# Kernel tuning notes

Hardware: AMD Instinct MI355X
Metric: run time of the kernel (lower is better)

## Reference

```python
import jax, jax.numpy as jnp
import numpy as np

B, S, D, H = 2, 2048, 1024, 16
HD = D // H  # 64


def setup_inputs() -> dict:
    key = jax.random.key(0)
    ks = jax.random.split(key, 10)
    sc = 1.0 / np.sqrt(D)
    return {
        "decoder_hs": jax.random.normal(ks[0], (B, S, D), jnp.float32),
        "encoder_hs": jax.random.normal(ks[1], (B, S, D), jnp.float32),
        "Wq": jax.random.normal(ks[2], (D, D), jnp.float32) * sc,
        "bq": jax.random.normal(ks[3], (D,), jnp.float32) * 0.02,
        "Wk": jax.random.normal(ks[4], (D, D), jnp.float32) * sc,
        "bk": jax.random.normal(ks[5], (D,), jnp.float32) * 0.02,
        "Wv": jax.random.normal(ks[6], (D, D), jnp.float32) * sc,
        "bv": jax.random.normal(ks[7], (D,), jnp.float32) * 0.02,
        "Wp": jax.random.normal(ks[8], (D, D), jnp.float32) * sc,
        "bp": jax.random.normal(ks[9], (D,), jnp.float32) * 0.02,
    }


def reference(decoder_hs, encoder_hs, Wq, bq, Wk, bk, Wv, bv, Wp, bp):
    b, s, d = decoder_hs.shape
    # torch nn.Linear: y = x @ W.T + b, W is [out, in]
    q = decoder_hs @ Wq.T + bq
    k = encoder_hs @ Wk.T + bk
    v = encoder_hs @ Wv.T + bv
    # head split: [b, s, d] -> [b, h, s, hd]
    q = q.reshape(b, s, H, HD).transpose(0, 2, 1, 3)
    k = k.reshape(b, s, H, HD).transpose(0, 2, 1, 3)
    v = v.reshape(b, s, H, HD).transpose(0, 2, 1, 3)
    scale = 1.0 / np.sqrt(HD).astype(np.float32)
    att = jnp.einsum('bhqd,bhkd->bhqk', q, k) * scale
    att = jax.nn.softmax(att, axis=-1)
    y = jnp.einsum('bhqk,bhkd->bhqd', att, v)
    y = y.transpose(0, 2, 1, 3).reshape(b, s, d)
    return y @ Wp.T + bp
```

## Files before the change

kernel.cpp:

```cpp
#include <hip/hip_runtime.h>
#include <hip/hip_bf16.h>
#include <cstdint>
#include <cstddef>

#define BB 2
#define SS 2048
#define DD 1024
#define HH 16
#define HD 64

typedef __attribute__((ext_vector_type(8))) short bf16x8;
typedef __attribute__((ext_vector_type(4))) float f32x4;
typedef __attribute__((ext_vector_type(16))) float f32x16;

#define GLL(g, l) __builtin_amdgcn_global_load_lds( \
    (const __attribute__((address_space(1))) void*)(g), \
    (__attribute__((address_space(3))) void*)(l), 16, 0, 0)

__device__ __forceinline__ short f2bf_fast(float f) {
    uint32_t u = __float_as_uint(f);
    u += 0x7FFF + ((u >> 16) & 1);
    return (short)(u >> 16);
}
__device__ __forceinline__ uint32_t pack_bf2(float a, float b) {
    uint32_t ua = __float_as_uint(a), ub = __float_as_uint(b);
    ua += 0x7FFF + ((ua >> 16) & 1);
    ub += 0x7FFF + ((ub >> 16) & 1);
    return (ua >> 16) | (ub & 0xFFFF0000u);
}
__device__ __forceinline__ uint32_t cvtpk_bf2(float a, float b) {
    uint32_t r;
    asm("v_cvt_pk_bf16_f32 %0, %1, %2" : "=v"(r) : "v"(a), "v"(b));
    return r;
}
__device__ __forceinline__ void pl32swap(uint32_t& a, uint32_t& b) {
    asm("v_permlane32_swap_b32 %0, %1" : "+v"(a), "+v"(b));
}
__device__ __forceinline__ bf16x8 cvt8(const float* __restrict__ p) {
    float4 a = *(const float4*)p;
    float4 b = *(const float4*)(p + 4);
    union { uint32_t d[4]; bf16x8 v; } r;
    r.d[0] = pack_bf2(a.x, a.y);
    r.d[1] = pack_bf2(a.z, a.w);
    r.d[2] = pack_bf2(b.x, b.y);
    r.d[3] = pack_bf2(b.z, b.w);
    return r.v;
}

__global__ __launch_bounds__(256) void cvt6_kernel(
    const float* __restrict__ s0, const float* __restrict__ s1,
    const float* __restrict__ s2, const float* __restrict__ s3,
    const float* __restrict__ s4, const float* __restrict__ s5,
    short* __restrict__ d0, short* __restrict__ d1, short* __restrict__ d2,
    short* __restrict__ d3, short* __restrict__ d4, short* __restrict__ d5)
{
    const int id = blockIdx.x * 256 + threadIdx.x;
    const float* s; short* d; size_t off;
    if (id < 1048576) {
        int e = id >> 19;
        off = (size_t)(id & 524287) * 8;
        s = e ? s1 : s0;  d = e ? d1 : d0;
    } else {
        int j = id - 1048576;
        int w = j >> 17;
        off = (size_t)(j & 131071) * 8;
        s = (w == 0) ? s2 : (w == 1) ? s3 : (w == 2) ? s4 : s5;
        d = (w == 0) ? d2 : (w == 1) ? d3 : (w == 2) ? d4 : d5;
    }
    bf16x8 r = cvt8(s + off);
    *(uint4*)(d + off) = *(uint4*)&r;
}

template<int BF>
__global__ __launch_bounds__(256, 3) void qkv_gemm_kernel(
    const void* __restrict__ dec, const void* __restrict__ enc,
    const void* __restrict__ Wq, const void* __restrict__ Wk,
    const void* __restrict__ Wv,
    const float* __restrict__ bq, const float* __restrict__ bk,
    const float* __restrict__ bv,
    short* __restrict__ Qo, short* __restrict__ Ko, short* __restrict__ Vo)
{
    __shared__ short As[128 * 32];
    __shared__ short Bs[128 * 32];

    const int z = blockIdx.z;
    const void* Xv = (z == 0) ? dec : enc;
    const void* Wp_ = (z == 0) ? Wq : (z == 1) ? Wk : Wv;
    const float* bias = (z == 0) ? bq : (z == 1) ? bk : bv;
    short* Yo = (z == 0) ? Qo : (z == 1) ? Ko : Vo;
    const float qs = (z == 0) ? (0.125f * 1.44269504088896f) : 1.0f;

    const int t = threadIdx.x;
    const int lane = t & 63, wv = t >> 6;
    const int lr = lane & 15, quad = lane >> 4;
    const int wm = wv >> 1, wn = wv & 1;
    const int m0 = blockIdx.y * 128;
    const int n0 = blockIdx.x * 128;
    const int K = DD;

    f32x4 acc[4][4];
    #pragma unroll
    for (int i = 0; i < 4; i++)
        #pragma unroll
        for (int j = 0; j < 4; j++) acc[i][j] = (f32x4){0.f, 0.f, 0.f, 0.f};

    for (int kb = 0; kb < K; kb += 32) {
        __syncthreads();
        if (BF) {
            const short* Xb = (const short*)Xv;
            const short* Wb = (const short*)Wp_;
            #pragma unroll
            for (int c = 0; c < 2; c++) {
                int r0 = wv * 32 + c * 16;
                int r = r0 + (lane >> 2), ch = (lane & 3) * 8;
                GLL(Xb + (size_t)(m0 + r) * K + kb + ch, &As[r0 * 32]);
                GLL(Wb + (size_t)(n0 + r) * K + kb + ch, &Bs[r0 * 32]);
            }
        } else {
            const float* Xf = (const float*)Xv;
            const float* Wf = (const float*)Wp_;
            #pragma unroll
            for (int c = 0; c < 2; c++) {
                int id = t + c * 256;
                int r = id >> 2, c8 = (id & 3) * 8;
                *(bf16x8*)&As[r * 32 + c8] = cvt8(Xf + (size_t)(m0 + r) * K + kb + c8);
                *(bf16x8*)&Bs[r * 32 + c8] = cvt8(Wf + (size_t)(n0 + r) * K + kb + c8);
            }
        }
        __syncthreads();

        bf16x8 af[4], bfr[4];
        #pragma unroll
        for (int mi = 0; mi < 4; mi++)
            af[mi] = *(const bf16x8*)&As[(wm * 64 + mi * 16 + lr) * 32 + quad * 8];
        #pragma unroll
        for (int ni = 0; ni < 4; ni++)
            bfr[ni] = *(const bf16x8*)&Bs[(wn * 64 + ni * 16 + lr) * 32 + quad * 8];
        #pragma unroll
        for (int mi = 0; mi < 4; mi++)
            #pragma unroll
            for (int ni = 0; ni < 4; ni++)
                acc[mi][ni] = __builtin_amdgcn_mfma_f32_16x16x32_bf16(
                    af[mi], bfr[ni], acc[mi][ni], 0, 0, 0);
    }

    if (z < 2) {
        #pragma unroll
        for (int ni = 0; ni < 4; ni++) {
            int col = n0 + wn * 64 + ni * 16 + lr;
            int h = col >> 6, hd = col & 63;
            float bvv = bias[col];
            #pragma unroll
            for (int mi = 0; mi < 4; mi++) {
                #pragma unroll
                for (int r2 = 0; r2 < 4; r2++) {
                    int row = m0 + wm * 64 + mi * 16 + quad * 4 + r2;
                    int b = row >> 11, s = row & 2047;
                    float v = (acc[mi][ni][r2] + bvv) * qs;
                    size_t off = ((size_t)(b * HH + h) * SS + s) * HD + hd;
                    Yo[off] = f2bf_fast(v);
                }
            }
        }
    } else {
        #pragma unroll
        for (int ni = 0; ni < 4; ni++) {
            int col = n0 + wn * 64 + ni * 16 + lr;
            int h = col >> 6, hd = col & 63;
            float bvv = bias[col];
            #pragma unroll
            for (int mi = 0; mi < 4; mi++) {
                int s0 = m0 + wm * 64 + mi * 16 + quad * 4;
                int b = s0 >> 11, s = s0 & 2047;
                union { uint32_t d[2]; } u;
                u.d[0] = pack_bf2(acc[mi][ni][0] + bvv, acc[mi][ni][1] + bvv);
                u.d[1] = pack_bf2(acc[mi][ni][2] + bvv, acc[mi][ni][3] + bvv);
                size_t off = ((size_t)(b * HH + h) * HD + hd) * SS + s;
                *(uint2*)(Yo + off) = *(uint2*)&u;
            }
        }
    }
}

template<int WBF>
__global__ __launch_bounds__(256, 2) void proj_gemm_kernel(
    const short* __restrict__ X,
    const void* __restrict__ W, const float* __restrict__ bias,
    float* __restrict__ Y)
{
    __shared__ short As[64 * 32];
    __shared__ short Bs[128 * 32];

    const int t = threadIdx.x;
    const int lane = t & 63, wv = t >> 6;
    const int lr = lane & 15, quad = lane >> 4;
    const int wm = wv >> 1, wn = wv & 1;
    const int m0 = blockIdx.y * 64;
    const int n0 = blockIdx.x * 128;
    const int K = DD, N = DD;

    f32x4 acc[2][4];
    #pragma unroll
    for (int i = 0; i < 2; i++)
        #pragma unroll
        for (int j = 0; j < 4; j++) acc[i][j] = (f32x4){0.f, 0.f, 0.f, 0.f};

    for (int kb = 0; kb < K; kb += 32) {
        __syncthreads();
        {
            int r0 = wv * 16;
            int r = r0 + (lane >> 2), ch = (lane & 3) * 8;
            GLL(X + (size_t)(m0 + r) * K + kb + ch, &As[r0 * 32]);
        }
        if (WBF) {
            const short* Wb = (const short*)W;
            #pragma unroll
            for (int c = 0; c < 2; c++) {
                int r0 = wv * 32 + c * 16;
                int r = r0 + (lane >> 2), ch = (lane & 3) * 8;
                GLL(Wb + (size_t)(n0 + r) * K + kb + ch, &Bs[r0 * 32]);
            }
        } else {
            const float* Wf = (const float*)W;
            #pragma unroll
            for (int c = 0; c < 2; c++) {
                int id = t + c * 256;
                int r = id >> 2, c8 = (id & 3) * 8;
                *(bf16x8*)&Bs[r * 32 + c8] = cvt8(Wf + (size_t)(n0 + r) * K + kb + c8);
            }
        }
        __syncthreads();

        bf16x8 af[2], bfr[4];
        #pragma unroll
        for (int mi = 0; mi < 2; mi++)
            af[mi] = *(const bf16x8*)&As[(wm * 32 + mi * 16 + lr) * 32 + quad * 8];
        #pragma unroll
        for (int ni = 0; ni < 4; ni++)
            bfr[ni] = *(const bf16x8*)&Bs[(wn * 64 + ni * 16 + lr) * 32 + quad * 8];
        #pragma unroll
        for (int mi = 0; mi < 2; mi++)
            #pragma unroll
            for (int ni = 0; ni < 4; ni++)
                acc[mi][ni] = __builtin_amdgcn_mfma_f32_16x16x32_bf16(
                    af[mi], bfr[ni], acc[mi][ni], 0, 0, 0);
    }

    #pragma unroll
    for (int ni = 0; ni < 4; ni++) {
        int col = n0 + wn * 64 + ni * 16 + lr;
        float bvv = bias[col];
        #pragma unroll
        for (int mi = 0; mi < 2; mi++) {
            #pragma unroll
            for (int r2 = 0; r2 < 4; r2++) {
                int row = m0 + wm * 32 + mi * 16 + quad * 4 + r2;
                Y[(size_t)row * N + col] = acc[mi][ni][r2] + bvv;
            }
        }
    }
}

__global__ __launch_bounds__(256, 2) void attn_kernel(
    const short* __restrict__ Q,
    const short* __restrict__ Kgl,
    const short* __restrict__ Vt_g,
    short* __restrict__ Y)
{
    __shared__ short Ks[2][128][64];
    __shared__ short Vt[2][64][128];

    const int t = threadIdx.x;
    const int lane = t & 63, w = t >> 6;
    const int lq = lane & 31, hf = lane >> 5;
    const int gl = (lq & 7) ^ ((lq >> 3) & 3);

    const int bid = blockIdx.x;
    const int slot = bid >> 3;
    const int bh = ((slot >> 4) << 3) + (bid & 7);
    const int qt = slot & 15;
    const int b = bh >> 4, h = bh & 15;

    const int q = qt * 128 + w * 32 + lq;
    const short* Qp = Q + ((size_t)bh * SS + q) * HD;
    bf16x8 qf[4];
    #pragma unroll
    for (int j = 0; j < 4; j++)
        qf[j] = *(const bf16x8*)(Qp + j * 16 + hf * 8);

    f32x16 o[2];
    #pragma unroll
    for (int i = 0; i < 16; i++) { o[0][i] = 0.f; o[1][i] = 0.f; }
    f32x4 vsum = (f32x4){0.f, 0.f, 0.f, 0.f};

    const short* Kb = Kgl + (size_t)bh * SS * HD;
    const short* Vb = Vt_g + (size_t)bh * HD * SS;

    auto stage = [&](int kt1, int nb) {
        #pragma unroll
        for (int c = 0; c < 4; c++) {
            int r0 = w * 32 + c * 8;
            int r  = r0 + (lane >> 3);
            int g  = (r & 7) ^ ((r >> 3) & 3);
            int sc = ((lane & 7) ^ g) * 8;
            GLL(Kb + (size_t)(kt1 * 128 + r) * 64 + sc, &Ks[nb][r0][0]);
        }
        #pragma unroll
        for (int c = 0; c < 4; c++) {
            int h0 = w * 16 + c * 4;
            int hd = h0 + (lane >> 4);
            int g  = (hd & 7) ^ ((hd >> 3) & 3);
            int s16 = (lane & 15) ^ g;
            GLL(Vb + (size_t)hd * SS + kt1 * 128 + s16 * 8, &Vt[nb][h0][0]);
        }
    };

    stage(0, 0);
    __syncthreads();

    int cur = 0;
    for (int kt = 0; kt < SS / 128; kt++) {
        if (kt + 1 < SS / 128) stage(kt + 1, cur ^ 1);

        bf16x8 pb[4][2];
        #pragma unroll
        for (int s = 0; s < 4; s++) {
            const short* krow = &Ks[cur][s * 32 + lq][0];
            f32x16 sc = (f32x16){0.f,0.f,0.f,0.f,0.f,0.f,0.f,0.f,
                                 0.f,0.f,0.f,0.f,0.f,0.f,0.f,0.f};
            __builtin_amdgcn_s_setprio(1);
            #pragma unroll
            for (int j = 0; j < 4; j++) {
                bf16x8 kf = *(const bf16x8*)&krow[((j * 2 + hf) ^ gl) * 8];
                sc = __builtin_amdgcn_mfma_f32_32x32x16_bf16(kf, qf[j], sc, 0, 0, 0);
            }
            __builtin_amdgcn_s_setprio(0);

            float ev[16];
            #pragma unroll
            for (int i = 0; i < 16; i++) ev[i] = __builtin_amdgcn_exp2f(sc[i]);
            #pragma unroll
            for (int r = 0; r < 4; r++)
                vsum += (f32x4){ev[4*r], ev[4*r+1], ev[4*r+2], ev[4*r+3]};
            uint32_t dw[8];
            #pragma unroll
            for (int i = 0; i < 8; i++) dw[i] = cvtpk_bf2(ev[2*i], ev[2*i+1]);
            pl32swap(dw[0], dw[2]); pl32swap(dw[1], dw[3]);
            pl32swap(dw[4], dw[6]); pl32swap(dw[5], dw[7]);
            union { uint32_t u[4]; bf16x8 v; } f0, f1;
            f0.u[0] = dw[0]; f0.u[1] = dw[1]; f0.u[2] = dw[2]; f0.u[3] = dw[3];
            f1.u[0] = dw[4]; f1.u[1] = dw[5]; f1.u[2] = dw[6]; f1.u[3] = dw[7];
            pb[s][0] = f0.v; pb[s][1] = f1.v;
        }

        __builtin_amdgcn_s_setprio(1);
        #pragma unroll
        for (int ds = 0; ds < 2; ds++) {
            const short* vrow = &Vt[cur][ds * 32 + lq][0];
            #pragma unroll
            for (int s = 0; s < 4; s++)
                #pragma unroll
                for (int c = 0; c < 2; c++) {
                    bf16x8 va = *(const bf16x8*)&vrow[((s * 4 + c * 2 + hf) ^ gl) * 8];
                    o[ds] = __builtin_amdgcn_mfma_f32_32x32x16_bf16(
                        va, pb[s][c], o[ds], 0, 0, 0);
                }
        }
        __builtin_amdgcn_s_setprio(0);

        __syncthreads();
        cur ^= 1;
    }

    float lsum = (vsum[0] + vsum[1]) + (vsum[2] + vsum[3]);
    lsum += __shfl_xor(lsum, 32, 64);
    float inv = 1.0f / lsum;

    short* Yp = Y + ((size_t)b * SS + q) * DD + h * 64 + hf * 4;
    #pragma unroll
    for (int ds = 0; ds < 2; ds++)
        #pragma unroll
        for (int rr = 0; rr < 4; rr++) {
            union { uint32_t d[2]; } u;
            u.d[0] = pack_bf2(o[ds][rr*4+0] * inv, o[ds][rr*4+1] * inv);
            u.d[1] = pack_bf2(o[ds][rr*4+2] * inv, o[ds][rr*4+3] * inv);
            *(uint2*)(Yp + ds * 32 + rr * 8) = *(uint2*)&u;
        }
}

extern "C" void kernel_launch(void* const* d_in, const int* in_sizes, int n_in,
                              void* d_out, int out_size, void* d_ws, size_t ws_size,
                              hipStream_t stream) {
    const float* dec = (const float*)d_in[0];
    const float* enc = (const float*)d_in[1];
    const float* Wq  = (const float*)d_in[2];
    const float* bq  = (const float*)d_in[3];
    const float* Wk  = (const float*)d_in[4];
    const float* bk  = (const float*)d_in[5];
    const float* Wv  = (const float*)d_in[6];
    const float* bv  = (const float*)d_in[7];
    const float* Wp  = (const float*)d_in[8];
    const float* bp  = (const float*)d_in[9];

    const size_t per = (size_t)BB * HH * SS * HD;
    const size_t wsz = (size_t)DD * DD;
    short* ws = (short*)d_ws;
    short* Qb  = ws;
    short* Kb  = ws + per;
    short* Vtb = ws + 2 * per;
    short* Yb  = ws + 3 * per;

    dim3 qkv_grid(DD / 128, (BB * SS) / 128, 3);
    dim3 proj_grid(DD / 128, (BB * SS) / 64);
    const int attn_blocks = BB * HH * (SS / 128);
    const int cvt_blocks = (2 * 524288 + 4 * 131072) / 256;

    const size_t need = (6 * per + 4 * wsz) * sizeof(short);
    if (ws_size >= need) {
        short* decb = ws + 4 * per;
        short* encb = ws + 5 * per;
        short* Wqb  = ws + 6 * per;
        short* Wkb  = Wqb + wsz;
        short* Wvb  = Wqb + 2 * wsz;
        short* Wpb  = Wqb + 3 * wsz;
        cvt6_kernel<<<cvt_blocks, 256, 0, stream>>>(
            dec, enc, Wq, Wk, Wv, Wp, decb, encb, Wqb, Wkb, Wvb, Wpb);
        qkv_gemm_kernel<1><<<qkv_grid, 256, 0, stream>>>(
            decb, encb, Wqb, Wkb, Wvb, bq, bk, bv, Qb, Kb, Vtb);
        attn_kernel<<<attn_blocks, 256, 0, stream>>>(Qb, Kb, Vtb, Yb);
        proj_gemm_kernel<1><<<proj_grid, 256, 0, stream>>>(Yb, Wpb, bp, (float*)d_out);
    } else {
        qkv_gemm_kernel<0><<<qkv_grid, 256, 0, stream>>>(
            dec, enc, Wq, Wk, Wv, bq, bk, bv, Qb, Kb, Vtb);
        attn_kernel<<<attn_blocks, 256, 0, stream>>>(Qb, Kb, Vtb, Yb);
        proj_gemm_kernel<0><<<proj_grid, 256, 0, stream>>>(Yb, Wp, bp, (float*)d_out);
    }
}
```

Before: 202.8 us.

## Split attention KV sequence across two wave groups per block with LDS reduction

The attention block grows to 512 threads: two groups of four waves each process half of the key/value sequence (1024 keys) for the same 128 queries, using 64-key tiles in separate LDS buffers. At the end the second group writes its partial output accumulators and row sums to LDS, and the first group adds them, normalizes and stores. This doubles the waves available per query tile to hide latency and raises occupancy. The cost is an extra LDS reduction, smaller tiles with more barriers, and tighter register limits under the new launch bounds.

```diff
diff --git a/kernel.cpp b/kernel.cpp
--- a/kernel.cpp
+++ b/kernel.cpp
@@ -261,17 +261,17 @@
     }
 }
 
-__global__ __launch_bounds__(256, 2) void attn_kernel(
+__global__ __launch_bounds__(512, 4) void attn_kernel(
     const short* __restrict__ Q,
     const short* __restrict__ Kgl,
     const short* __restrict__ Vt_g,
     short* __restrict__ Y)
 {
-    __shared__ short Ks[2][128][64];
-    __shared__ short Vt[2][64][128];
+    __shared__ short smem[32768];
 
     const int t = threadIdx.x;
     const int lane = t & 63, w = t >> 6;
+    const int h2 = w >> 2, qw = w & 3;
     const int lq = lane & 31, hf = lane >> 5;
     const int gl = (lq & 7) ^ ((lq >> 3) & 3);
 
@@ -281,7 +281,7 @@
     const int qt = slot & 15;
     const int b = bh >> 4, h = bh & 15;
 
-    const int q = qt * 128 + w * 32 + lq;
+    const int q = qt * 128 + qw * 32 + lq;
     const short* Qp = Q + ((size_t)bh * SS + q) * HD;
     bf16x8 qf[4];
     #pragma unroll
@@ -293,25 +293,29 @@
     for (int i = 0; i < 16; i++) { o[0][i] = 0.f; o[1][i] = 0.f; }
     f32x4 vsum = (f32x4){0.f, 0.f, 0.f, 0.f};
 
-    const short* Kb = Kgl + (size_t)bh * SS * HD;
-    const short* Vb = Vt_g + (size_t)bh * HD * SS;
+    const short* Kb = Kgl + ((size_t)bh * SS + h2 * 1024) * HD;
+    const short* Vb = Vt_g + (size_t)bh * HD * SS + h2 * 1024;
+
+    short* KT[2] = { smem + (h2 * 2 + 0) * 4096, smem + (h2 * 2 + 1) * 4096 };
+    short* VT[2] = { smem + 16384 + (h2 * 2 + 0) * 4096,
+                     smem + 16384 + (h2 * 2 + 1) * 4096 };
 
     auto stage = [&](int kt1, int nb) {
         #pragma unroll
-        for (int c = 0; c < 4; c++) {
-            int r0 = w * 32 + c * 8;
+        for (int c = 0; c < 2; c++) {
+            int r0 = qw * 16 + c * 8;
             int r  = r0 + (lane >> 3);
             int g  = (r & 7) ^ ((r >> 3) & 3);
             int sc = ((lane & 7) ^ g) * 8;
-            GLL(Kb + (size_t)(kt1 * 128 + r) * 64 + sc, &Ks[nb][r0][0]);
-        }
-        #pragma unroll
-        for (int c = 0; c < 4; c++) {
-            int h0 = w * 16 + c * 4;
-            int hd = h0 + (lane >> 4);
+            GLL(Kb + (size_t)(kt1 * 64 + r) * HD + sc, KT[nb] + r0 * 64);
+        }
+        #pragma unroll
+        for (int c = 0; c < 2; c++) {
+            int h0 = qw * 16 + c * 8;
+            int hd = h0 + (lane >> 3);
             int g  = (hd & 7) ^ ((hd >> 3) & 3);
-            int s16 = (lane & 15) ^ g;
-            GLL(Vb + (size_t)hd * SS + kt1 * 128 + s16 * 8, &Vt[nb][h0][0]);
+            int s8 = (lane & 7) ^ g;
+            GLL(Vb + (size_t)hd * SS + kt1 * 64 + s8 * 8, VT[nb] + h0 * 64);
         }
     };
 
@@ -319,13 +323,13 @@
     __syncthreads();
 
     int cur = 0;
-    for (int kt = 0; kt < SS / 128; kt++) {
-        if (kt + 1 < SS / 128) stage(kt + 1, cur ^ 1);
-
-        bf16x8 pb[4][2];
-        #pragma unroll
-        for (int s = 0; s < 4; s++) {
-            const short* krow = &Ks[cur][s * 32 + lq][0];
+    for (int kt = 0; kt < 16; kt++) {
+        if (kt < 15) stage(kt + 1, cur ^ 1);
+
+        bf16x8 pb[2][2];
+        #pragma unroll
+        for (int s = 0; s < 2; s++) {
+            const short* krow = KT[cur] + (s * 32 + lq) * 64;
             f32x16 sc = (f32x16){0.f,0.f,0.f,0.f,0.f,0.f,0.f,0.f,
                                  0.f,0.f,0.f,0.f,0.f,0.f,0.f,0.f};
             __builtin_amdgcn_s_setprio(1);
@@ -356,9 +360,9 @@
         __builtin_amdgcn_s_setprio(1);
         #pragma unroll
         for (int ds = 0; ds < 2; ds++) {
-            const short* vrow = &Vt[cur][ds * 32 + lq][0];
-            #pragma unroll
-            for (int s = 0; s < 4; s++)
+            const short* vrow = VT[cur] + (ds * 32 + lq) * 64;
+            #pragma unroll
+            for (int s = 0; s < 2; s++)
                 #pragma unroll
                 for (int c = 0; c < 2; c++) {
                     bf16x8 va = *(const bf16x8*)&vrow[((s * 4 + c * 2 + hf) ^ gl) * 8];
@@ -374,18 +378,33 @@
 
     float lsum = (vsum[0] + vsum[1]) + (vsum[2] + vsum[3]);
     lsum += __shfl_xor(lsum, 32, 64);
-    float inv = 1.0f / lsum;
-
-    short* Yp = Y + ((size_t)b * SS + q) * DD + h * 64 + hf * 4;
-    #pragma unroll
-    for (int ds = 0; ds < 2; ds++)
-        #pragma unroll
-        for (int rr = 0; rr < 4; rr++) {
-            union { uint32_t d[2]; } u;
-            u.d[0] = pack_bf2(o[ds][rr*4+0] * inv, o[ds][rr*4+1] * inv);
-            u.d[1] = pack_bf2(o[ds][rr*4+2] * inv, o[ds][rr*4+3] * inv);
-            *(uint2*)(Yp + ds * 32 + rr * 8) = *(uint2*)&u;
-        }
+
+    float* xb = (float*)smem;
+    if (h2) {
+        float* p = xb + ((size_t)(qw * 64 + lane)) * 33;
+        #pragma unroll
+        for (int i = 0; i < 16; i++) { p[i] = o[0][i]; p[16 + i] = o[1][i]; }
+        p[32] = lsum;
+    }
+    __syncthreads();
+    if (!h2) {
+        const float* p = xb + ((size_t)(qw * 64 + lane)) * 33;
+        #pragma unroll
+        for (int i = 0; i < 16; i++) { o[0][i] += p[i]; o[1][i] += p[16 + i]; }
+        lsum += p[32];
+        float inv = 1.0f / lsum;
+
+        short* Yp = Y + ((size_t)b * SS + q) * DD + h * 64 + hf * 4;
+        #pragma unroll
+        for (int ds = 0; ds < 2; ds++)
+            #pragma unroll
+            for (int rr = 0; rr < 4; rr++) {
+                union { uint32_t d[2]; } u;
+                u.d[0] = pack_bf2(o[ds][rr*4+0] * inv, o[ds][rr*4+1] * inv);
+                u.d[1] = pack_bf2(o[ds][rr*4+2] * inv, o[ds][rr*4+3] * inv);
+                *(uint2*)(Yp + ds * 32 + rr * 8) = *(uint2*)&u;
+            }
+    }
 }
 
 extern "C" void kernel_launch(void* const* d_in, const int* in_sizes, int n_in,
@@ -427,12 +446,12 @@
             dec, enc, Wq, Wk, Wv, Wp, decb, encb, Wqb, Wkb, Wvb, Wpb);
         qkv_gemm_kernel<1><<<qkv_grid, 256, 0, stream>>>(
             decb, encb, Wqb, Wkb, Wvb, bq, bk, bv, Qb, Kb, Vtb);
-        attn_kernel<<<attn_blocks, 256, 0, stream>>>(Qb, Kb, Vtb, Yb);
+        attn_kernel<<<attn_blocks, 512, 0, stream>>>(Qb, Kb, Vtb, Yb);
         proj_gemm_kernel<1><<<proj_grid, 256, 0, stream>>>(Yb, Wpb, bp, (float*)d_out);
     } else {
         qkv_gemm_kernel<0><<<qkv_grid, 256, 0, stream>>>(
             dec, enc, Wq, Wk, Wv, bq, bk, bv, Qb, Kb, Vtb);
-        attn_kernel<<<attn_blocks, 256, 0, stream>>>(Qb, Kb, Vtb, Yb);
+        attn_kernel<<<attn_blocks, 512, 0, stream>>>(Qb, Kb, Vtb, Yb);
         proj_gemm_kernel<0><<<proj_grid, 256, 0, stream>>>(Yb, Wp, bp, (float*)d_out);
     }
 }
```

After: 207.1 us. 2.1% more time.
